# Kernel optimization log

Measured on AMD Instinct MI355X. Metric: run time of the kernel, lower is better.

The kernel has to match this reference:

```python
import jax, jax.numpy as jnp
import numpy as np

EMBED_DIM = 512
B, N = 8, 2048


def setup_inputs() -> dict:
    key = jax.random.key(0)
    ks = jax.random.split(key, 9)
    d = EMBED_DIM
    s = 1.0 / np.sqrt(d)
    return {
        "x": jax.random.normal(ks[0], (B, N, d), dtype=jnp.float32),
        "Wq": jax.random.uniform(ks[1], (d, d), jnp.float32, -s, s),
        "bq": jax.random.uniform(ks[2], (d,), jnp.float32, -s, s),
        "Wk": jax.random.uniform(ks[3], (d, d), jnp.float32, -s, s),
        "bk": jax.random.uniform(ks[4], (d,), jnp.float32, -s, s),
        "Wv": jax.random.uniform(ks[5], (d, d), jnp.float32, -s, s),
        "bv": jax.random.uniform(ks[6], (d,), jnp.float32, -s, s),
        "Wo": jax.random.uniform(ks[7], (d, d), jnp.float32, -s, s),
        "bo": jax.random.uniform(ks[8], (d,), jnp.float32, -s, s),
    }


def reference(x, Wq, bq, Wk, bk, Wv, bv, Wo, bo):
    d = x.shape[-1]
    scale = d ** (-0.5)
    q = x @ Wq + bq              # [B, N, D]
    k = x @ Wk + bk
    v = x @ Wv + bv
    attn = jnp.einsum('bnd,bmd->bnm', q, k) * scale  # [B, N, N]
    attn = jax.nn.softmax(attn, axis=-1)
    out = jnp.einsum('bnm,bmd->bnd', attn, v)
    return out @ Wo + bo
```

## Files before the change

kernel.cpp:

```cpp
#include <hip/hip_runtime.h>
#include <hip/hip_bf16.h>
#include <hip/hip_fp8.h>
#include <stdint.h>

typedef __bf16 bf16;
typedef __attribute__((ext_vector_type(8))) short short8;
typedef __attribute__((ext_vector_type(4))) float f32x4;
typedef __attribute__((ext_vector_type(4))) bf16 bf16x4;

#define DIM 512
#define NBATCH 8
#define SEQ 2048

__device__ __forceinline__ void gld_lds16(const void* g, void* l) {
    __builtin_amdgcn_global_load_lds(
        (const __attribute__((address_space(1))) void*)g,
        (__attribute__((address_space(3))) void*)l,
        16, 0, 0);
}

__device__ __forceinline__ unsigned char f32_to_e4m3(float v) {
#if __has_builtin(__builtin_amdgcn_cvt_pk_fp8_f32)
    return (unsigned char)(__builtin_amdgcn_cvt_pk_fp8_f32(v, v, 0, false) & 0xff);
#else
    return __hip_cvt_float_to_fp8(v, __HIP_SATFINITE, __HIP_E4M3);
#endif
}

template <int MODE, int SWIZ>
__global__ __launch_bounds__(256) void gemm_bt(
    const bf16* __restrict__ A, const bf16* __restrict__ Bt,
    void* __restrict__ Cv, const float* __restrict__ bias,
    int N, int K, long long sC, float alpha, int gx)
{
    __shared__ bf16 smem[32768];
    bf16* Asb = smem;
    bf16* Bsb = smem + 16384;

    int bx, by;
    {
        const unsigned g = blockIdx.x;
        const unsigned xcd = g & 7;
        const unsigned t = g >> 3;
        const unsigned per = (gridDim.x >> 3) / (unsigned)gx;
        by = xcd * per + t / (unsigned)gx;
        bx = t % (unsigned)gx;
    }

    const int tid  = threadIdx.x;
    const int lane = tid & 63;
    const int w    = tid >> 6;
    const int wr   = w >> 1;
    const int wc   = w & 1;
    const int lm   = lane & 15;
    const int lk   = lane >> 4;
    const int fs   = lm & 7;
    const int rq   = tid >> 3;
    const int pc   = tid & 7;
    const int scol = ((pc ^ (rq & 7)) * 8);

    const bf16* Ag = A + (size_t)(by * 128) * K;
    const bf16* Bg = Bt + (size_t)(bx * 128) * K;

    f32x4 acc[4][4];
#pragma unroll
    for (int i = 0; i < 4; ++i)
#pragma unroll
        for (int j = 0; j < 4; ++j)
            acc[i][j] = (f32x4){0.f, 0.f, 0.f, 0.f};

    auto stage = [&](int kb, int buf) {
#pragma unroll
        for (int t = 0; t < 4; ++t) {
            const int r = t * 32 + rq;
            gld_lds16(Ag + (size_t)r * K + kb + scol,
                      Asb + buf * 8192 + t * 2048 + tid * 8);
            gld_lds16(Bg + (size_t)r * K + kb + scol,
                      Bsb + buf * 8192 + t * 2048 + tid * 8);
        }
    };
    auto compute = [&](int buf) {
        const bf16* Ab = Asb + buf * 8192;
        const bf16* Bb = Bsb + buf * 8192;
#pragma unroll
        for (int s = 0; s < 2; ++s) {
            const int u = ((s * 4 + lk) ^ fs) * 8;
            short8 fa[4], fb[4];
#pragma unroll
            for (int i = 0; i < 4; ++i)
                fa[i] = *(const short8*)&Ab[(wr * 64 + i * 16 + lm) * 64 + u];
#pragma unroll
            for (int j = 0; j < 4; ++j)
                fb[j] = *(const short8*)&Bb[(wc * 64 + j * 16 + lm) * 64 + u];
#pragma unroll
            for (int i = 0; i < 4; ++i)
#pragma unroll
                for (int j = 0; j < 4; ++j)
                    acc[i][j] = __builtin_amdgcn_mfma_f32_16x16x32_bf16(
                        fa[i], fb[j], acc[i][j], 0, 0, 0);
        }
    };

    stage(0, 0);
    __syncthreads();
    const int E = K >> 6;
#pragma unroll 2
    for (int e = 0; e < E; ++e) {
        if (e + 1 < E) stage((e + 1) << 6, (e + 1) & 1);
        compute(e & 1);
        __syncthreads();
    }

    if (MODE == 2) {
        float* ft = (float*)smem;
        float* outp = (float*)Cv;
#pragma unroll
        for (int h = 0; h < 2; ++h) {
            if (wr == h) {
#pragma unroll
                for (int i = 0; i < 4; ++i)
#pragma unroll
                    for (int j = 0; j < 4; ++j) {
                        const int col = wc * 64 + j * 16 + lm;
                        const float bv = bias[bx * 128 + col];
#pragma unroll
                        for (int r = 0; r < 4; ++r)
                            ft[(i * 16 + lk * 4 + r) * 132 + col] =
                                acc[i][j][r] + bv;
                    }
            }
            __syncthreads();
            const int rr = tid >> 5, cc = (tid & 31) * 4;
#pragma unroll
            for (int p = 0; p < 8; ++p) {
                const int row = p * 8 + rr;
                *(float4*)&outp[(size_t)(by * 128 + h * 64 + row) * N +
                                bx * 128 + cc] = *(const float4*)&ft[row * 132 + cc];
            }
            __syncthreads();
        }
        return;
    }

#pragma unroll
    for (int i = 0; i < 4; ++i)
#pragma unroll
        for (int j = 0; j < 4; ++j) {
            const int col = bx * 128 + wc * 64 + j * 16 + lm;
            const float bv = bias[col];
#pragma unroll
            for (int r = 0; r < 4; ++r)
                acc[i][j][r] += bv;
        }

    const int sub = (bx * 128) >> 9;
    bf16* dst = (bf16*)Cv + (size_t)sub * 8388608;
    const int col0 = (bx * 128) & 511;
#pragma unroll
    for (int h = 0; h < 2; ++h) {
        if (wr == h) {
#pragma unroll
            for (int i = 0; i < 4; ++i)
#pragma unroll
                for (int j = 0; j < 4; ++j)
#pragma unroll
                    for (int r = 0; r < 4; ++r)
                        smem[(i * 16 + lk * 4 + r) * 136 + wc * 64 + j * 16 + lm] =
                            (bf16)acc[i][j][r];
        }
        __syncthreads();
        const int rr0 = tid >> 4, cc = (tid & 15) * 8;
#pragma unroll
        for (int p = 0; p < 4; ++p) {
            const int row = p * 16 + rr0;
            const uint4 raw = *(const uint4*)&smem[row * 136 + cc];
            *(uint4*)&dst[(size_t)(by * 128 + h * 64 + row) * 512 + col0 + cc] = raw;
        }
        __syncthreads();
    }
}

template <int MODE>
__global__ __launch_bounds__(256) void gemm_f8(
    const uint8_t* __restrict__ A, const uint8_t* __restrict__ Bt,
    void* __restrict__ Cv, float* __restrict__ rsum,
    int N, int K, long long sA, long long sB, long long sC, float alpha,
    int gx)
{
    __shared__ uint8_t smem[32768];
    uint8_t* As = smem;
    uint8_t* Bs = smem + 16384;

    int bx, by, bz;
    {
        const unsigned g = blockIdx.x;
        bz = g & 7;
        const unsigned r = g >> 3;
        bx = r % (unsigned)gx;
        by = r / (unsigned)gx;
    }

    const int tid  = threadIdx.x;
    const int lane = tid & 63;
    const int w    = tid >> 6;
    const int wr   = w >> 1;
    const int wc   = w & 1;
    const int lm   = lane & 15;
    const int lk   = lane >> 4;
    const int rq   = tid >> 3;
    const int pc   = tid & 7;
    const int ssrc = (pc ^ (rq & 7)) * 16;

    const size_t z = bz;
    const uint8_t* Ag = A + z * (size_t)sA + (size_t)(by * 128) * K;
    const uint8_t* Bg = Bt + z * (size_t)sB + (size_t)(bx * 128) * K;

    f32x4 acc[4][4];
#pragma unroll
    for (int i = 0; i < 4; ++i)
#pragma unroll
        for (int j = 0; j < 4; ++j)
            acc[i][j] = (f32x4){0.f, 0.f, 0.f, 0.f};

    for (int kb = 0; kb < K; kb += 128) {
#pragma unroll
        for (int t = 0; t < 4; ++t) {
            const int r = t * 32 + rq;
            gld_lds16(Ag + (size_t)r * K + kb + ssrc, As + t * 4096 + tid * 16);
            gld_lds16(Bg + (size_t)r * K + kb + ssrc, Bs + t * 4096 + tid * 16);
        }
        __syncthreads();

#pragma unroll
        for (int s = 0; s < 4; ++s) {
            const int h = s * 4 + lk;
            long long fa[4], fb[4];
#pragma unroll
            for (int i = 0; i < 4; ++i) {
                const int row = wr * 64 + i * 16 + lm;
                fa[i] = *(const long long*)&As[row * 128 +
                        (((h >> 1) ^ (row & 7)) * 16) + (h & 1) * 8];
            }
#pragma unroll
            for (int j = 0; j < 4; ++j) {
                const int row = wc * 64 + j * 16 + lm;
                fb[j] = *(const long long*)&Bs[row * 128 +
                        (((h >> 1) ^ (row & 7)) * 16) + (h & 1) * 8];
            }
#pragma unroll
            for (int i = 0; i < 4; ++i)
#pragma unroll
                for (int j = 0; j < 4; ++j)
                    acc[i][j] = __builtin_amdgcn_mfma_f32_16x16x32_fp8_fp8(
                        fa[i], fb[j], acc[i][j], 0, 0, 0);
        }
        __syncthreads();
    }

    const int orow0 = by * 128 + wr * 64;

    if (MODE == 4) {
#pragma unroll
        for (int i = 0; i < 4; ++i) {
            float psum[4] = {0.f, 0.f, 0.f, 0.f};
#pragma unroll
            for (int j = 0; j < 4; ++j)
#pragma unroll
                for (int r = 0; r < 4; ++r) {
                    const float e = __expf(acc[i][j][r] * alpha);
                    acc[i][j][r] = e;
                    psum[r] += e;
                }
#pragma unroll
            for (int m = 1; m < 16; m <<= 1)
#pragma unroll
                for (int r = 0; r < 4; ++r) psum[r] += __shfl_xor(psum[r], m);
            if (lm == 0) {
#pragma unroll
                for (int r = 0; r < 4; ++r)
                    atomicAdd(&rsum[z * SEQ + orow0 + i * 16 + lk * 4 + r],
                              psum[r]);
            }
        }
        uint8_t* dst = (uint8_t*)Cv + z * (size_t)sC;
#pragma unroll
        for (int h = 0; h < 2; ++h) {
            if (wr == h) {
#pragma unroll
                for (int i = 0; i < 4; ++i)
#pragma unroll
                    for (int j = 0; j < 4; ++j)
#pragma unroll
                        for (int r = 0; r < 4; ++r)
                            smem[(i * 16 + lk * 4 + r) * 144 +
                                 wc * 64 + j * 16 + lm] =
                                f32_to_e4m3(acc[i][j][r]);
            }
            __syncthreads();
            const int rr = tid >> 3, cc = (tid & 7) * 16;
#pragma unroll
            for (int p = 0; p < 2; ++p) {
                const int row = p * 32 + rr;
                const uint4 raw = *(const uint4*)&smem[row * 144 + cc];
                *(uint4*)&dst[(size_t)(by * 128 + h * 64 + row) * N +
                              bx * 128 + cc] = raw;
            }
            __syncthreads();
        }
        return;
    }

#pragma unroll
    for (int i = 0; i < 4; ++i) {
        float inv[4];
#pragma unroll
        for (int r = 0; r < 4; ++r)
            inv[r] = 1.0f / (32.0f * rsum[z * SEQ + orow0 + i * 16 + lk * 4 + r]);
#pragma unroll
        for (int j = 0; j < 4; ++j)
#pragma unroll
            for (int r = 0; r < 4; ++r)
                acc[i][j][r] *= inv[r];
    }
    bf16* dst = (bf16*)Cv + z * (size_t)sC;
    bf16* tile = (bf16*)smem;
#pragma unroll
    for (int h = 0; h < 2; ++h) {
        if (wr == h) {
#pragma unroll
            for (int i = 0; i < 4; ++i)
#pragma unroll
                for (int j = 0; j < 4; ++j)
#pragma unroll
                    for (int r = 0; r < 4; ++r)
                        tile[(i * 16 + lk * 4 + r) * 136 + wc * 64 + j * 16 + lm] =
                            (bf16)acc[i][j][r];
        }
        __syncthreads();
        const int rr0 = tid >> 4, cc = (tid & 15) * 8;
#pragma unroll
        for (int p = 0; p < 4; ++p) {
            const int row = p * 16 + rr0;
            const uint4 raw = *(const uint4*)&tile[row * 136 + cc];
            *(uint4*)&dst[(size_t)(by * 128 + h * 64 + row) * N + bx * 128 + cc] =
                raw;
        }
        __syncthreads();
    }
}

__global__ __launch_bounds__(256) void transpose_v(
    const bf16* __restrict__ V, uint8_t* __restrict__ Vt)
{
    __shared__ bf16 tile[64][72];
    const int b = blockIdx.z, tx = blockIdx.x, ty = blockIdx.y;
    const int t0 = threadIdx.x;
#pragma unroll
    for (int it = 0; it < 2; ++it) {
        const int idx = it * 256 + t0;
        const int r = idx >> 3, c0 = (idx & 7) * 8;
        const uint4 raw = *(const uint4*)&V[((size_t)b * SEQ + ty * 64 + r) * 512 +
                                            tx * 64 + c0];
        const bf16* v8 = (const bf16*)&raw;
#pragma unroll
        for (int j = 0; j < 8; ++j) tile[c0 + j][r] = v8[j];
    }
    __syncthreads();
#pragma unroll
    for (int it = 0; it < 2; ++it) {
        const int idx = it * 256 + t0;
        const int o = idx >> 3, i0 = (idx & 7) * 8;
        uint2 pk;
        uint8_t* pb = (uint8_t*)&pk;
#pragma unroll
        for (int j = 0; j < 8; ++j)
            pb[j] = f32_to_e4m3(32.0f * (float)tile[o][i0 + j]);
        *(uint2*)&Vt[((size_t)b * 512 + tx * 64 + o) * SEQ + ty * 64 + i0] = pk;
    }
}

__global__ __launch_bounds__(256) void cvt_bf16_f8(
    const bf16* __restrict__ in, uint8_t* __restrict__ out, int n8)
{
    const int i = blockIdx.x * 256 + threadIdx.x;
    if (i >= n8) return;
    const uint4 raw = ((const uint4*)in)[i];
    const bf16* v = (const bf16*)&raw;
    uint2 pk;
    uint8_t* pb = (uint8_t*)&pk;
#pragma unroll
    for (int j = 0; j < 8; ++j)
        pb[j] = f32_to_e4m3(32.0f * (float)v[j]);
    ((uint2*)out)[i] = pk;
}

__global__ __launch_bounds__(256) void cvt_f32_bf16(
    const float* __restrict__ x, bf16* __restrict__ o, int n4)
{
    const int i = blockIdx.x * 256 + threadIdx.x;
    if (i >= n4) return;
    const float4 v = ((const float4*)x)[i];
    bf16x4 b;
    b[0] = (bf16)v.x; b[1] = (bf16)v.y; b[2] = (bf16)v.z; b[3] = (bf16)v.w;
    ((bf16x4*)o)[i] = b;
}

__global__ __launch_bounds__(256) void transpose4(
    const float* __restrict__ Wq, const float* __restrict__ Wk,
    const float* __restrict__ Wv, const float* __restrict__ Wo,
    bf16* __restrict__ Wcat, bf16* __restrict__ Wto,
    const float* __restrict__ bq, const float* __restrict__ bk,
    const float* __restrict__ bv, float* __restrict__ bcat,
    float* __restrict__ rowsum)
{
    const int widx = blockIdx.z;
    const int t0 = threadIdx.x;
    if (widx == 4) {
        const int idx = (blockIdx.y * 8 + blockIdx.x) * 256 + t0;
        rowsum[idx] = 0.0f;
        if (idx < 1536)
            bcat[idx] = (idx < 512) ? bq[idx]
                      : (idx < 1024) ? bk[idx - 512] : bv[idx - 1024];
        return;
    }
    __shared__ bf16 tile[64][65];
    const float* W = (widx == 0) ? Wq : (widx == 1) ? Wk : (widx == 2) ? Wv : Wo;
    bf16* dst = (widx < 3) ? (Wcat + (size_t)widx * 512 * 512) : Wto;
    const int tx = blockIdx.x, ty = blockIdx.y;
#pragma unroll
    for (int it = 0; it < 16; ++it) {
        const int e = it * 256 + t0;
        const int r = e >> 6, c = e & 63;
        tile[r][c] = (bf16)W[(size_t)(ty * 64 + r) * 512 + tx * 64 + c];
    }
    __syncthreads();
#pragma unroll
    for (int it = 0; it < 16; ++it) {
        const int e = it * 256 + t0;
        const int o = e >> 6, i = e & 63;
        dst[(size_t)(tx * 64 + o) * 512 + ty * 64 + i] = tile[i][o];
    }
}

extern "C" void kernel_launch(void* const* d_in, const int* in_sizes, int n_in,
                              void* d_out, int out_size, void* d_ws, size_t ws_size,
                              hipStream_t stream)
{
    const float* x  = (const float*)d_in[0];
    const float* Wq = (const float*)d_in[1];
    const float* bq = (const float*)d_in[2];
    const float* Wk = (const float*)d_in[3];
    const float* bk = (const float*)d_in[4];
    const float* Wv = (const float*)d_in[5];
    const float* bv = (const float*)d_in[6];
    const float* Wo = (const float*)d_in[7];
    const float* bo = (const float*)d_in[8];
    float* out = (float*)d_out;

    char* ws = (char*)d_ws;
    bf16*    Xb     = (bf16*)(ws);
    bf16*    Ctx    = (bf16*)(ws);
    bf16*    Wcat   = (bf16*)(ws + 16777216);
    bf16*    Wto    = (bf16*)(ws + 18350080);
    float*   bcat   = (float*)(ws + 18874368);
    float*   rowsum = (float*)(ws + 18880512);
    bf16*    Q      = (bf16*)(ws + 20971520);
    uint8_t* Q8     = (uint8_t*)(ws + 71303168);
    uint8_t* Vt8    = (uint8_t*)(ws + 88080384);
    uint8_t* S8     = (uint8_t*)(ws + 96468992);

    transpose4<<<dim3(8, 8, 5), 256, 0, stream>>>(
        Wq, Wk, Wv, Wo, Wcat, Wto, bq, bk, bv, bcat, rowsum);
    cvt_f32_bf16<<<8192, 256, 0, stream>>>(x, Xb, 2097152);

    const float scale = 0.044194173824159216f;

    gemm_bt<3, 2><<<1536, 256, 0, stream>>>(
        Xb, Wcat, Q, bcat, 1536, 512, 0, 1.0f, 12);

    cvt_bf16_f8<<<8192, 256, 0, stream>>>(Q, Q8, 2097152);
    transpose_v<<<dim3(8, 32, 8), 256, 0, stream>>>(Q + 16777216, Vt8);

    gemm_f8<4><<<2048, 256, 0, stream>>>(
        Q8, Q8 + 8388608, S8, rowsum, 2048, 512,
        2048LL * 512, 2048LL * 512, 2048LL * 2048, scale / 1024.0f, 16);

    gemm_f8<5><<<512, 256, 0, stream>>>(
        S8, Vt8, Ctx, rowsum, 512, 2048,
        2048LL * 2048, 512LL * 2048, 2048LL * 512, 1.0f, 4);

    gemm_bt<2, 2><<<512, 256, 0, stream>>>(
        Ctx, Wto, out, bo, 512, 512, 0, 1.0f, 4);
}
```

Before: 256.2 us.

## Use MX-scaled 16x16x128 fp8 MFMA and fuse fp8 quantization into QKV epilogue

The fp8 GEMMs for QK^T and PV switch from the 16x16x32 fp8 MFMA to the gfx950 scaled 16x16x128 f8f6f4 MFMA with unit scales. Each wave now loads 32-byte fragments per row and issues a quarter as many MFMA instructions per K-block. Separately, the QKV projection epilogue writes Q and K directly as fp8 (and V as bf16), which removes the standalone bf16-to-fp8 conversion kernel and its extra pass over memory. The risks are correctness of the new fragment layout and LDS swizzle indexing, and the workspace layout being remapped.

```diff
diff --git a/kernel.cpp b/kernel.cpp
--- a/kernel.cpp
+++ b/kernel.cpp
@@ -7,6 +7,8 @@
 typedef __attribute__((ext_vector_type(8))) short short8;
 typedef __attribute__((ext_vector_type(4))) float f32x4;
 typedef __attribute__((ext_vector_type(4))) bf16 bf16x4;
+typedef __attribute__((ext_vector_type(8))) int int8v;
+typedef __attribute__((ext_vector_type(4))) int int4v;
 
 #define DIM 512
 #define NBATCH 8
@@ -153,35 +155,65 @@
                 acc[i][j][r] += bv;
         }
 
-    const int sub = (bx * 128) >> 9;
-    bf16* dst = (bf16*)Cv + (size_t)sub * 8388608;
+    const int sub  = (bx * 128) >> 9;
     const int col0 = (bx * 128) & 511;
-#pragma unroll
-    for (int h = 0; h < 2; ++h) {
-        if (wr == h) {
-#pragma unroll
-            for (int i = 0; i < 4; ++i)
-#pragma unroll
-                for (int j = 0; j < 4; ++j)
-#pragma unroll
-                    for (int r = 0; r < 4; ++r)
-                        smem[(i * 16 + lk * 4 + r) * 136 + wc * 64 + j * 16 + lm] =
-                            (bf16)acc[i][j][r];
-        }
-        __syncthreads();
-        const int rr0 = tid >> 4, cc = (tid & 15) * 8;
-#pragma unroll
-        for (int p = 0; p < 4; ++p) {
-            const int row = p * 16 + rr0;
-            const uint4 raw = *(const uint4*)&smem[row * 136 + cc];
-            *(uint4*)&dst[(size_t)(by * 128 + h * 64 + row) * 512 + col0 + cc] = raw;
-        }
-        __syncthreads();
+
+    if (sub < 2) {
+        uint8_t* d8 = (uint8_t*)Cv + (size_t)sub * 8388608;
+        uint8_t* t8 = (uint8_t*)smem;
+#pragma unroll
+        for (int h = 0; h < 2; ++h) {
+            if (wr == h) {
+#pragma unroll
+                for (int i = 0; i < 4; ++i)
+#pragma unroll
+                    for (int j = 0; j < 4; ++j)
+#pragma unroll
+                        for (int r = 0; r < 4; ++r)
+                            t8[(i * 16 + lk * 4 + r) * 144 + wc * 64 + j * 16 + lm] =
+                                f32_to_e4m3(32.0f * acc[i][j][r]);
+            }
+            __syncthreads();
+            const int rr = tid >> 3, cc = (tid & 7) * 16;
+#pragma unroll
+            for (int p = 0; p < 2; ++p) {
+                const int row = p * 32 + rr;
+                const uint4 raw = *(const uint4*)&t8[row * 144 + cc];
+                *(uint4*)&d8[(size_t)(by * 128 + h * 64 + row) * 512 + col0 + cc] =
+                    raw;
+            }
+            __syncthreads();
+        }
+    } else {
+        bf16* dst = (bf16*)((uint8_t*)Cv + 16777216);
+#pragma unroll
+        for (int h = 0; h < 2; ++h) {
+            if (wr == h) {
+#pragma unroll
+                for (int i = 0; i < 4; ++i)
+#pragma unroll
+                    for (int j = 0; j < 4; ++j)
+#pragma unroll
+                        for (int r = 0; r < 4; ++r)
+                            smem[(i * 16 + lk * 4 + r) * 136 + wc * 64 + j * 16 + lm] =
+                                (bf16)acc[i][j][r];
+            }
+            __syncthreads();
+            const int rr0 = tid >> 4, cc = (tid & 15) * 8;
+#pragma unroll
+            for (int p = 0; p < 4; ++p) {
+                const int row = p * 16 + rr0;
+                const uint4 raw = *(const uint4*)&smem[row * 136 + cc];
+                *(uint4*)&dst[(size_t)(by * 128 + h * 64 + row) * 512 + col0 + cc] =
+                    raw;
+            }
+            __syncthreads();
+        }
     }
 }
 
 template <int MODE>
-__global__ __launch_bounds__(256) void gemm_f8(
+__global__ __launch_bounds__(256) void gemm_mx(
     const uint8_t* __restrict__ A, const uint8_t* __restrict__ Bt,
     void* __restrict__ Cv, float* __restrict__ rsum,
     int N, int K, long long sA, long long sB, long long sC, float alpha,
@@ -210,6 +242,8 @@
     const int rq   = tid >> 3;
     const int pc   = tid & 7;
     const int ssrc = (pc ^ (rq & 7)) * 16;
+    const int ca   = ((2 * lk) ^ (lm & 7)) * 16;
+    const int cb   = ((2 * lk + 1) ^ (lm & 7)) * 16;
 
     const size_t z = bz;
     const uint8_t* Ag = A + z * (size_t)sA + (size_t)(by * 128) * K;
@@ -231,28 +265,25 @@
         }
         __syncthreads();
 
-#pragma unroll
-        for (int s = 0; s < 4; ++s) {
-            const int h = s * 4 + lk;
-            long long fa[4], fb[4];
-#pragma unroll
-            for (int i = 0; i < 4; ++i) {
-                const int row = wr * 64 + i * 16 + lm;
-                fa[i] = *(const long long*)&As[row * 128 +
-                        (((h >> 1) ^ (row & 7)) * 16) + (h & 1) * 8];
-            }
-#pragma unroll
-            for (int j = 0; j < 4; ++j) {
-                const int row = wc * 64 + j * 16 + lm;
-                fb[j] = *(const long long*)&Bs[row * 128 +
-                        (((h >> 1) ^ (row & 7)) * 16) + (h & 1) * 8];
-            }
+        int8v fa[4];
+#pragma unroll
+        for (int i = 0; i < 4; ++i) {
+            const uint8_t* rp = As + (wr * 64 + i * 16 + lm) * 128;
+            const int4v lo = *(const int4v*)(rp + ca);
+            const int4v hi = *(const int4v*)(rp + cb);
+            fa[i] = (int8v){lo[0], lo[1], lo[2], lo[3], hi[0], hi[1], hi[2], hi[3]};
+        }
+#pragma unroll
+        for (int j = 0; j < 4; ++j) {
+            const uint8_t* rp = Bs + (wc * 64 + j * 16 + lm) * 128;
+            const int4v lo = *(const int4v*)(rp + ca);
+            const int4v hi = *(const int4v*)(rp + cb);
+            const int8v fb = (int8v){lo[0], lo[1], lo[2], lo[3],
+                                     hi[0], hi[1], hi[2], hi[3]};
 #pragma unroll
             for (int i = 0; i < 4; ++i)
-#pragma unroll
-                for (int j = 0; j < 4; ++j)
-                    acc[i][j] = __builtin_amdgcn_mfma_f32_16x16x32_fp8_fp8(
-                        fa[i], fb[j], acc[i][j], 0, 0, 0);
+                acc[i][j] = __builtin_amdgcn_mfma_scale_f32_16x16x128_f8f6f4(
+                    fa[i], fb, acc[i][j], 0, 0, 0, 127, 0, 127);
         }
         __syncthreads();
     }
@@ -377,21 +408,6 @@
             pb[j] = f32_to_e4m3(32.0f * (float)tile[o][i0 + j]);
         *(uint2*)&Vt[((size_t)b * 512 + tx * 64 + o) * SEQ + ty * 64 + i0] = pk;
     }
-}
-
-__global__ __launch_bounds__(256) void cvt_bf16_f8(
-    const bf16* __restrict__ in, uint8_t* __restrict__ out, int n8)
-{
-    const int i = blockIdx.x * 256 + threadIdx.x;
-    if (i >= n8) return;
-    const uint4 raw = ((const uint4*)in)[i];
-    const bf16* v = (const bf16*)&raw;
-    uint2 pk;
-    uint8_t* pb = (uint8_t*)&pk;
-#pragma unroll
-    for (int j = 0; j < 8; ++j)
-        pb[j] = f32_to_e4m3(32.0f * (float)v[j]);
-    ((uint2*)out)[i] = pk;
 }
 
 __global__ __launch_bounds__(256) void cvt_f32_bf16(
@@ -464,10 +480,11 @@
     bf16*    Wto    = (bf16*)(ws + 18350080);
     float*   bcat   = (float*)(ws + 18874368);
     float*   rowsum = (float*)(ws + 18880512);
-    bf16*    Q      = (bf16*)(ws + 20971520);
-    uint8_t* Q8     = (uint8_t*)(ws + 71303168);
-    uint8_t* Vt8    = (uint8_t*)(ws + 88080384);
-    uint8_t* S8     = (uint8_t*)(ws + 96468992);
+    uint8_t* Q8     = (uint8_t*)(ws + 20971520);
+    uint8_t* K8     = (uint8_t*)(ws + 29360128);
+    bf16*    V      = (bf16*)(ws + 37748736);
+    uint8_t* Vt8    = (uint8_t*)(ws + 54525952);
+    uint8_t* S8     = (uint8_t*)(ws + 62914560);
 
     transpose4<<<dim3(8, 8, 5), 256, 0, stream>>>(
         Wq, Wk, Wv, Wo, Wcat, Wto, bq, bk, bv, bcat, rowsum);
@@ -476,16 +493,15 @@
     const float scale = 0.044194173824159216f;
 
     gemm_bt<3, 2><<<1536, 256, 0, stream>>>(
-        Xb, Wcat, Q, bcat, 1536, 512, 0, 1.0f, 12);
-
-    cvt_bf16_f8<<<8192, 256, 0, stream>>>(Q, Q8, 2097152);
-    transpose_v<<<dim3(8, 32, 8), 256, 0, stream>>>(Q + 16777216, Vt8);
-
-    gemm_f8<4><<<2048, 256, 0, stream>>>(
-        Q8, Q8 + 8388608, S8, rowsum, 2048, 512,
+        Xb, Wcat, Q8, bcat, 1536, 512, 0, 1.0f, 12);
+
+    transpose_v<<<dim3(8, 32, 8), 256, 0, stream>>>(V, Vt8);
+
+    gemm_mx<4><<<2048, 256, 0, stream>>>(
+        Q8, K8, S8, rowsum, 2048, 512,
         2048LL * 512, 2048LL * 512, 2048LL * 2048, scale / 1024.0f, 16);
 
-    gemm_f8<5><<<512, 256, 0, stream>>>(
+    gemm_mx<5><<<512, 256, 0, stream>>>(
         S8, Vt8, Ctx, rowsum, 512, 2048,
         2048LL * 2048, 512LL * 2048, 2048LL * 512, 1.0f, 4);
 
```

Result: faster. 226.2 us (-11.7%).
